# Performance work log

Hardware: AMD Instinct MI355X
Metric: run time of the kernel (lower is better)

## Reference

```python
import jax, jax.numpy as jnp
import numpy as np
import math

D_MODEL = 1024
N_HEADS = 16
D_HEAD = 64


def setup_inputs() -> dict:
    key = jax.random.key(0)
    ks = jax.random.split(key, 9)
    B, T = 2, 2048
    s = 1.0 / math.sqrt(D_MODEL)
    return {
        "x": jax.random.normal(ks[0], (B, T, D_MODEL), dtype=jnp.float32),
        "Wq": jax.random.normal(ks[1], (D_MODEL, D_MODEL), dtype=jnp.float32) * s,
        "bq": jnp.zeros((D_MODEL,), dtype=jnp.float32),
        "Wk": jax.random.normal(ks[2], (D_MODEL, D_MODEL), dtype=jnp.float32) * s,
        "bk": jnp.zeros((D_MODEL,), dtype=jnp.float32),
        "Wv": jax.random.normal(ks[3], (D_MODEL, D_MODEL), dtype=jnp.float32) * s,
        "bv": jnp.zeros((D_MODEL,), dtype=jnp.float32),
        "Wo": jax.random.normal(ks[4], (D_MODEL, D_MODEL), dtype=jnp.float32) * s,
        "bo": jnp.zeros((D_MODEL,), dtype=jnp.float32),
    }


def reference(x, Wq, bq, Wk, bk, Wv, bv, Wo, bo):
    B, T, _ = x.shape
    # Linear layers (torch convention: y = x @ W^T + b)
    Q = x @ Wq.T + bq
    K = x @ Wk.T + bk
    V = x @ Wv.T + bv
    # [B, H, T, Dh]
    Q = Q.reshape(B, T, N_HEADS, D_HEAD).transpose(0, 2, 1, 3)
    K = K.reshape(B, T, N_HEADS, D_HEAD).transpose(0, 2, 1, 3)
    V = V.reshape(B, T, N_HEADS, D_HEAD).transpose(0, 2, 1, 3)
    scores = jnp.einsum("bhqd,bhkd->bhqk", Q, K) / math.sqrt(D_HEAD)
    causal_mask = jnp.tril(jnp.ones((T, T), dtype=bool))  # [T, T]
    scores = jnp.where(causal_mask, scores, -jnp.inf)
    attn = jax.nn.softmax(scores, axis=-1)
    out = jnp.einsum("bhqk,bhkd->bhqd", attn, V)
    out = out.transpose(0, 2, 1, 3).reshape(B, T, D_MODEL)
    return out @ Wo.T + bo
```

## Files before the change

kernel.cpp:

```cpp
#include <hip/hip_runtime.h>

typedef unsigned short u16;
typedef __bf16 bf16x8 __attribute__((ext_vector_type(8)));
typedef float f32x4 __attribute__((ext_vector_type(4)));
typedef float f32x16 __attribute__((ext_vector_type(16)));
typedef u16 u16x4 __attribute__((ext_vector_type(4)));
typedef unsigned int uint;

#define DM 1024
#define MROWS 4096
#define TSEQ 2048

static __device__ __forceinline__ u16 f2b(float f) {
  uint u = __builtin_bit_cast(uint, f);
  uint r = (u + 0x7fffu + ((u >> 16) & 1u)) >> 16;
  return (u16)r;
}

static __device__ __forceinline__ uint pkbf(float a, float b) {
  union { __bf16 h[2]; uint u; } x;
  x.h[0] = (__bf16)a; x.h[1] = (__bf16)b;
  return x.u;
}

__global__ __launch_bounds__(256) void cvt_kernel(const float* __restrict__ in,
                                                  u16* __restrict__ out, int n,
                                                  float scale) {
  int i = (blockIdx.x * 256 + threadIdx.x) * 4;
  if (i >= n) return;
  float4 v = *(const float4*)(in + i);
  u16x4 o;
  o.x = f2b(v.x * scale); o.y = f2b(v.y * scale);
  o.z = f2b(v.z * scale); o.w = f2b(v.w * scale);
  *(u16x4*)(out + i) = o;
}

__global__ __launch_bounds__(256) void cvt4_kernel(
    const float* __restrict__ w0, const float* __restrict__ w1,
    const float* __restrict__ w2, const float* __restrict__ w3,
    u16* __restrict__ o0, u16* __restrict__ o1, u16* __restrict__ o2,
    u16* __restrict__ o3, float s0) {
  const int sel = blockIdx.y;
  const float* in = (sel == 0) ? w0 : (sel == 1) ? w1 : (sel == 2) ? w2 : w3;
  u16* out = (sel == 0) ? o0 : (sel == 1) ? o1 : (sel == 2) ? o2 : o3;
  const float scale = (sel == 0) ? s0 : 1.0f;
  int i = (blockIdx.x * 256 + threadIdx.x) * 4;
  float4 v = *(const float4*)(in + i);
  u16x4 o;
  o.x = f2b(v.x * scale); o.y = f2b(v.y * scale);
  o.z = f2b(v.z * scale); o.w = f2b(v.w * scale);
  *(u16x4*)(out + i) = o;
}

#define SWZ(o) ((o) ^ ((((o) >> 7) & 3) << 4))

static __device__ __forceinline__ void gemm_tile(const u16* __restrict__ A,
                                                 const u16* __restrict__ W,
                                                 int row0, int col0,
                                                 char* lds,
                                                 f32x4 (&acc)[4][4]) {
  const int tid = threadIdx.x;
  const int lane = tid & 63, wid = tid >> 6;
  const int wr = wid >> 1, wc = wid & 1;
  const int lg = lane >> 4, lr = lane & 15;

  const u16* srcA[2]; const u16* srcB[2]; int dst[2];
#pragma unroll
  for (int c = 0; c < 2; ++c) {
    int lin = (c * 256 + tid) * 16;
    int p = SWZ(lin);
    srcA[c] = A + (size_t)(row0 + (p >> 6)) * DM + ((p & 63) >> 1);
    srcB[c] = W + (size_t)(col0 + (p >> 6)) * DM + ((p & 63) >> 1);
    dst[c] = lin;
  }
  int offA[4], offB[4];
#pragma unroll
  for (int m = 0; m < 4; ++m) offA[m] = SWZ((wr * 64 + m * 16 + lr) * 64 + lg * 16);
#pragma unroll
  for (int n = 0; n < 4; ++n) offB[n] = SWZ((wc * 64 + n * 16 + lr) * 64 + lg * 16);

  f32x4 z = {0.f, 0.f, 0.f, 0.f};
#pragma unroll
  for (int m = 0; m < 4; ++m)
#pragma unroll
    for (int n = 0; n < 4; ++n) acc[m][n] = z;

  auto stage = [&](int k0, int buf) {
    char* bA = lds + buf * 16384;
    char* bB = bA + 8192;
#pragma unroll
    for (int c = 0; c < 2; ++c) {
      __builtin_amdgcn_global_load_lds(
          (const __attribute__((address_space(1))) void*)(srcA[c] + k0),
          (__attribute__((address_space(3))) void*)(bA + dst[c]), 16, 0, 0);
      __builtin_amdgcn_global_load_lds(
          (const __attribute__((address_space(1))) void*)(srcB[c] + k0),
          (__attribute__((address_space(3))) void*)(bB + dst[c]), 16, 0, 0);
    }
  };

  stage(0, 0);
  __syncthreads();
  int cur = 0;
  for (int k0 = 0; k0 < DM; k0 += 32) {
    if (k0 + 32 < DM) stage(k0 + 32, cur ^ 1);
    char* bA = lds + cur * 16384;
    char* bB = bA + 8192;
    bf16x8 av[4], bv[4];
#pragma unroll
    for (int m = 0; m < 4; ++m) av[m] = *(const bf16x8*)(bA + offA[m]);
#pragma unroll
    for (int n = 0; n < 4; ++n) bv[n] = *(const bf16x8*)(bB + offB[n]);
    __builtin_amdgcn_s_setprio(1);
#pragma unroll
    for (int m = 0; m < 4; ++m)
#pragma unroll
      for (int n = 0; n < 4; ++n)
        acc[m][n] = __builtin_amdgcn_mfma_f32_16x16x32_bf16(av[m], bv[n], acc[m][n], 0, 0, 0);
    __builtin_amdgcn_s_setprio(0);
    __syncthreads();
    cur ^= 1;
  }
}

__global__ __launch_bounds__(256) void qkv_gemm(
    const u16* __restrict__ xb, const u16* __restrict__ Wqb,
    const u16* __restrict__ Wkb, const u16* __restrict__ Wvb,
    const float* __restrict__ bq, const float* __restrict__ bk,
    const float* __restrict__ bv, u16* __restrict__ Qx, u16* __restrict__ Kx,
    u16* __restrict__ Vx) {
  __shared__ char lds[32768];
  const int seg = blockIdx.x >> 3, nt = blockIdx.x & 7;
  const int row0 = blockIdx.y * 128, col0 = nt * 128;
  const u16* W = (seg == 0) ? Wqb : (seg == 1) ? Wkb : Wvb;
  const float* bias = (seg == 0) ? bq : (seg == 1) ? bk : bv;
  const float bscale = (seg == 0) ? 0.18033688011112042f : 1.0f;

  f32x4 acc[4][4];
  gemm_tile(xb, W, row0, col0, lds, acc);

  const int tid = threadIdx.x;
  const int lane = tid & 63, wid = tid >> 6;
  const int wr = wid >> 1, wc = wid & 1;
  const int lg = lane >> 4, lr = lane & 15;

  float bcol[4];
#pragma unroll
  for (int n = 0; n < 4; ++n) bcol[n] = bias[col0 + wc * 64 + n * 16 + lr] * bscale;
#pragma unroll
  for (int m = 0; m < 4; ++m)
#pragma unroll
    for (int n = 0; n < 4; ++n) {
      int colB = (wc * 64 + n * 16 + lr) * 2;
#pragma unroll
      for (int r = 0; r < 4; ++r) {
        int row = wr * 64 + m * 16 + lg * 4 + r;
        *(u16*)(lds + row * 256 + (colB ^ ((row & 7) << 4))) =
            f2b(acc[m][n][r] + bcol[n]);
      }
    }
  __syncthreads();

  const int st = tid >> 5, lnq = tid & 31;
  const int bI = row0 >> 11;
  if (seg < 2) {
    u16* out = (seg == 0) ? Qx : Kx;
    const int hloc = st & 1, twloc = st >> 1;
    const int h = (col0 >> 6) + hloc;
    const int tw = ((row0 & 2047) >> 5) + twloc;
    u16* base = out + ((size_t)(bI * 16 + h) * 64 + tw) * 2048;
#pragma unroll
    for (int ch = 0; ch < 8; ++ch) {
      int q = ch * 256 + lnq * 8;
      int c = q >> 9, hi2 = (q >> 8) & 1;
      int row = twloc * 32 + lnq;
      int colB = hloc * 128 + c * 32 + hi2 * 16;
      bf16x8 v = *(const bf16x8*)(lds + row * 256 + (colB ^ ((row & 7) << 4)));
      *(bf16x8*)(base + q) = v;
    }
  } else {
    const int hloc = st & 1, ktloc = st >> 1;
    const int h = (col0 >> 6) + hloc;
    const int kt = ((row0 & 2047) >> 5) + ktloc;
    u16* base = Vx + ((size_t)(bI * 16 + h) * 64 + kt) * 2048;
#pragma unroll
    for (int ch = 0; ch < 8; ++ch) {
      int q = ch * 256 + lnq * 8;
      int hi2 = ch & 1, hh = (ch >> 1) & 1, c = (ch >> 2) & 1;
      int colB = (hloc * 64 + hh * 32 + lnq) * 2;
      union { u16 a[8]; bf16x8 v; } t;
#pragma unroll
      for (int j = 0; j < 8; ++j) {
        int kvi = 16 * c + (j & 3) + 8 * (j >> 2) + 4 * hi2;
        int row = ktloc * 32 + kvi;
        t.a[j] = *(const u16*)(lds + row * 256 + (colB ^ ((row & 7) << 4)));
      }
      *(bf16x8*)(base + q) = t.v;
    }
  }
}

__global__ __launch_bounds__(256, 4) void attn_kernel(const u16* __restrict__ Qx,
                                                      const u16* __restrict__ Kx,
                                                      const u16* __restrict__ Vx,
                                                      u16* __restrict__ Aout) {
  __shared__ u16 stg[2][2][4096];
  __shared__ float mml[2][64][2];
  const int tid = threadIdx.x, lane = tid & 63, wid = tid >> 6;
  const int hi = lane >> 5, ln = lane & 31;
  const int half = wid & 1, spl = wid >> 1;
  const int id = blockIdx.x + (blockIdx.y << 5);
  const int xcd = id & 7, idx = id >> 3;
  const int bh = xcd * 4 + (idx & 3);
  const int qt = 31 - (idx >> 2);
  const int b = bh >> 4, h = bh & 15;
  const int q0 = qt * 64 + half * 32;
  const int tbeg = spl * (qt + 1);
  const int tend = tbeg + (qt + 1);

  const u16* Qp = Qx + ((size_t)bh * 64 + (q0 >> 5)) * 2048;
  const u16* Kt = Kx + (size_t)bh * 64 * 2048;
  const u16* Vt = Vx + (size_t)bh * 64 * 2048;

  bf16x8 qf[4];
#pragma unroll
  for (int c = 0; c < 4; ++c)
    qf[c] = *(const bf16x8*)(Qp + c * 512 + hi * 256 + ln * 8);

  f32x16 Oa, Ob;
#pragma unroll
  for (int r = 0; r < 16; ++r) { Oa[r] = 0.f; Ob[r] = 0.f; }
  float m = -1e30f, l = 0.f;

  u16* myStg = &stg[spl][0][0];
  const u16* srcB = (half == 0) ? Kt : Vt;
  auto stage = [&](int kt, int s) {
    const u16* src = srcB + (size_t)kt * 2048;
    u16* dst = myStg + s * 4096 + half * 2048;
#pragma unroll
    for (int c = 0; c < 4; ++c)
      __builtin_amdgcn_global_load_lds(
          (const __attribute__((address_space(1))) void*)(src + c * 512 + lane * 8),
          (__attribute__((address_space(3))) void*)(dst + c * 512 + lane * 8),
          16, 0, 0);
  };

  stage(tbeg, 0);
  __syncthreads();
  for (int kt = tbeg; kt < tend; ++kt) {
    const int s = (kt - tbeg) & 1;
    if (kt + 1 < tend) stage(kt + 1, s ^ 1);
    const u16* Kl = myStg + s * 4096;
    const u16* Vl = Kl + 2048;
    bf16x8 kf[4], vf[4];
#pragma unroll
    for (int c = 0; c < 4; ++c)
      kf[c] = *(const bf16x8*)(Kl + c * 512 + hi * 256 + ln * 8);
#pragma unroll
    for (int c = 0; c < 4; ++c)
      vf[c] = *(const bf16x8*)(Vl + c * 512 + hi * 256 + ln * 8);
    f32x16 S;
#pragma unroll
    for (int r = 0; r < 16; ++r) S[r] = 0.f;
    __builtin_amdgcn_s_setprio(1);
#pragma unroll
    for (int c = 0; c < 4; ++c)
      S = __builtin_amdgcn_mfma_f32_32x32x16_bf16(kf[c], qf[c], S, 0, 0, 0);
    __builtin_amdgcn_s_setprio(0);
    if (kt >= (q0 >> 5)) {
      const int q = q0 + ln;
#pragma unroll
      for (int r = 0; r < 16; ++r) {
        int kv = kt * 32 + (r & 3) + 8 * (r >> 2) + 4 * hi;
        if (kv > q) S[r] = -1e38f;
      }
    }
    float a0 = fmaxf(fmaxf(S[0], S[1]), S[2]);
    float a1 = fmaxf(fmaxf(S[3], S[4]), S[5]);
    float a2 = fmaxf(fmaxf(S[6], S[7]), S[8]);
    float a3 = fmaxf(fmaxf(S[9], S[10]), S[11]);
    float a4 = fmaxf(fmaxf(S[12], S[13]), S[14]);
    float mx = fmaxf(fmaxf(fmaxf(a0, a1), fmaxf(a2, a3)), fmaxf(a4, S[15]));
    if (!__all(mx - m <= 8.f)) {
      float nm = fmaxf(m, mx);
      nm = fmaxf(nm, __shfl_xor(nm, 32));
      float sf = __builtin_amdgcn_exp2f(m - nm);
      m = nm; l *= sf;
#pragma unroll
      for (int r = 0; r < 16; ++r) { Oa[r] *= sf; Ob[r] *= sf; }
    }
#pragma unroll
    for (int r = 0; r < 16; ++r) S[r] = __builtin_amdgcn_exp2f(S[r] - m);
    float ts = ((S[0] + S[1]) + (S[2] + S[3])) + ((S[4] + S[5]) + (S[6] + S[7]));
    ts += ((S[8] + S[9]) + (S[10] + S[11])) + ((S[12] + S[13]) + (S[14] + S[15]));
    l += ts;
    uint pw[8];
#pragma unroll
    for (int i = 0; i < 8; ++i) pw[i] = pkbf(S[2 * i], S[2 * i + 1]);
    __builtin_amdgcn_s_setprio(1);
#pragma unroll
    for (int c = 0; c < 2; ++c) {
      union { uint w[4]; bf16x8 v; } pf;
      pf.w[0] = pw[4 * c + 0]; pf.w[1] = pw[4 * c + 1];
      pf.w[2] = pw[4 * c + 2]; pf.w[3] = pw[4 * c + 3];
      Oa = __builtin_amdgcn_mfma_f32_32x32x16_bf16(vf[2 * c + 0], pf.v, Oa, 0, 0, 0);
      Ob = __builtin_amdgcn_mfma_f32_32x32x16_bf16(vf[2 * c + 1], pf.v, Ob, 0, 0, 0);
    }
    __builtin_amdgcn_s_setprio(0);
    __syncthreads();
  }

  union uo { f32x16 v; f32x4 q[4]; };
  const int sw8 = lane & 7;
  char* moc = (char*)&stg[0][0][0] + half * 8192;
  if (spl == 1) {
    uo ua, ub; ua.v = Oa; ub.v = Ob;
#pragma unroll
    for (int c = 0; c < 4; ++c) {
      *(f32x4*)(moc + lane * 128 + ((c ^ sw8) * 16)) = ua.q[c];
      *(f32x4*)(moc + lane * 128 + (((c + 4) ^ sw8) * 16)) = ub.q[c];
    }
    mml[half][lane][0] = m;
    mml[half][lane][1] = l;
  }
  __syncthreads();
  if (spl == 1) return;

  {
    float mY = mml[half][lane][0], lY = mml[half][lane][1];
    f32x4 rb[8];
#pragma unroll
    for (int c = 0; c < 8; ++c)
      rb[c] = *(const f32x4*)(moc + lane * 128 + ((c ^ sw8) * 16));
    float M = fmaxf(m, mY);
    float eX = __builtin_amdgcn_exp2f(m - M);
    float eY = __builtin_amdgcn_exp2f(mY - M);
    uo ua, ub; ua.v = Oa; ub.v = Ob;
#pragma unroll
    for (int c = 0; c < 4; ++c) {
      ua.q[c] = ua.q[c] * eX + rb[c] * eY;
      ub.q[c] = ub.q[c] * eX + rb[c + 4] * eY;
    }
    Oa = ua.v; Ob = ub.v;
    l = l * eX + lY * eY;
  }

  float lr = l + __shfl_xor(l, 32);
  const float inv = 1.f / lr;

  __threadfence_block();
  char* Tc = moc;
#pragma unroll
  for (int i = 0; i < 8; ++i) {
    int d0 = (2 * i & 3) + 8 * ((2 * i) >> 2) + 4 * hi;
    uint wA = pkbf(Oa[2 * i] * inv, Oa[2 * i + 1] * inv);
    *(uint*)(Tc + (ln * 128 + ((d0 * 2) ^ ((ln & 7) << 4)))) = wA;
    uint wB = pkbf(Ob[2 * i] * inv, Ob[2 * i + 1] * inv);
    *(uint*)(Tc + (ln * 128 + (((d0 + 32) * 2) ^ ((ln & 7) << 4)))) = wB;
  }
  __threadfence_block();
  u16* Ap = Aout + (size_t)b * TSEQ * DM + h * 64 + (size_t)(q0 + ln) * DM;
#pragma unroll
  for (int j = 0; j < 4; ++j) {
    int oct = hi * 4 + j;
    bf16x8 v = *(const bf16x8*)(Tc + (ln * 128 + ((oct * 16) ^ ((ln & 7) << 4))));
    *(bf16x8*)(Ap + oct * 8) = v;
  }
}

__global__ __launch_bounds__(256) void out_gemm(const u16* __restrict__ attn,
                                                const u16* __restrict__ Wob,
                                                const float* __restrict__ bo,
                                                float* __restrict__ out) {
  __shared__ char lds[32768];
  const int row0 = blockIdx.y * 128, col0 = blockIdx.x * 128;
  f32x4 acc[4][4];
  gemm_tile(attn, Wob, row0, col0, lds, acc);

  const int tid = threadIdx.x;
  const int lane = tid & 63, wid = tid >> 6;
  const int wr = wid >> 1, wc = wid & 1;
  const int lg = lane >> 4, lr = lane & 15;
#pragma unroll
  for (int m = 0; m < 4; ++m)
#pragma unroll
    for (int n = 0; n < 4; ++n) {
      int col = col0 + wc * 64 + n * 16 + lr;
      float b = bo[col];
#pragma unroll
      for (int r = 0; r < 4; ++r) {
        int row = row0 + wr * 64 + m * 16 + lg * 4 + r;
        out[(size_t)row * DM + col] = acc[m][n][r] + b;
      }
    }
}

extern "C" void kernel_launch(void* const* d_in, const int* in_sizes, int n_in,
                              void* d_out, int out_size, void* d_ws, size_t ws_size,
                              hipStream_t stream) {
  const float* x = (const float*)d_in[0];
  const float* Wq = (const float*)d_in[1];
  const float* bq = (const float*)d_in[2];
  const float* Wk = (const float*)d_in[3];
  const float* bk = (const float*)d_in[4];
  const float* Wv = (const float*)d_in[5];
  const float* bv = (const float*)d_in[6];
  const float* Wo = (const float*)d_in[7];
  const float* bo = (const float*)d_in[8];

  char* ws = (char*)d_ws;
  const size_t MB = 1024 * 1024;
  u16* xb = (u16*)(ws);
  u16* Wqb = (u16*)(ws + 8 * MB);
  u16* Wkb = (u16*)(ws + 10 * MB);
  u16* Wvb = (u16*)(ws + 12 * MB);
  u16* Wob = (u16*)(ws + 14 * MB);
  u16* Qf = (u16*)(ws + 16 * MB);
  u16* Kf = (u16*)(ws + 24 * MB);
  u16* Vf = (u16*)(ws + 32 * MB);
  u16* attnb = xb;

  cvt_kernel<<<4096, 256, 0, stream>>>(x, xb, MROWS * DM, 1.0f);
  cvt4_kernel<<<dim3(1024, 4), 256, 0, stream>>>(Wq, Wk, Wv, Wo, Wqb, Wkb, Wvb,
                                                 Wob, 0.18033688011112042f);

  qkv_gemm<<<dim3(24, 32), 256, 0, stream>>>(xb, Wqb, Wkb, Wvb, bq, bk, bv, Qf, Kf, Vf);
  attn_kernel<<<dim3(32, 32), 256, 0, stream>>>(Qf, Kf, Vf, attnb);
  out_gemm<<<dim3(8, 32), 256, 0, stream>>>(attnb, Wob, bo, (float*)d_out);
}
```

Before: 101.0 us.

## Merge conversion kernels, vectorize V transpose, and register-prefetch K/V in attention

The two fp32-to-bf16 conversion launches become one kernel, removing a launch. In the QKV GEMM epilogue, V is written to LDS directly in its transposed, swizzled layout so the scattered 2-byte reads become single 16-byte reads. The attention kernel drops the shared LDS staging and per-tile __syncthreads, and instead loads K and V tiles straight into registers with double-buffered K prefetch. It also splits the KV range per 32-row half rather than per 64-row tile, which balances causal work and applies the mask only on the diagonal tile, at the cost of more register pressure and uncoalesced-reuse global loads.

```diff
diff --git a/kernel.cpp b/kernel.cpp
--- a/kernel.cpp
+++ b/kernel.cpp
@@ -23,28 +23,23 @@
   return x.u;
 }
 
-__global__ __launch_bounds__(256) void cvt_kernel(const float* __restrict__ in,
-                                                  u16* __restrict__ out, int n,
-                                                  float scale) {
-  int i = (blockIdx.x * 256 + threadIdx.x) * 4;
-  if (i >= n) return;
-  float4 v = *(const float4*)(in + i);
-  u16x4 o;
-  o.x = f2b(v.x * scale); o.y = f2b(v.y * scale);
-  o.z = f2b(v.z * scale); o.w = f2b(v.w * scale);
-  *(u16x4*)(out + i) = o;
-}
-
-__global__ __launch_bounds__(256) void cvt4_kernel(
-    const float* __restrict__ w0, const float* __restrict__ w1,
-    const float* __restrict__ w2, const float* __restrict__ w3,
-    u16* __restrict__ o0, u16* __restrict__ o1, u16* __restrict__ o2,
-    u16* __restrict__ o3, float s0) {
-  const int sel = blockIdx.y;
-  const float* in = (sel == 0) ? w0 : (sel == 1) ? w1 : (sel == 2) ? w2 : w3;
-  u16* out = (sel == 0) ? o0 : (sel == 1) ? o1 : (sel == 2) ? o2 : o3;
-  const float scale = (sel == 0) ? s0 : 1.0f;
-  int i = (blockIdx.x * 256 + threadIdx.x) * 4;
+__global__ __launch_bounds__(256) void cvt_all(
+    const float* __restrict__ x, const float* __restrict__ w0,
+    const float* __restrict__ w1, const float* __restrict__ w2,
+    const float* __restrict__ w3, u16* __restrict__ xo, u16* __restrict__ o0,
+    u16* __restrict__ o1, u16* __restrict__ o2, u16* __restrict__ o3,
+    float s0) {
+  const int bid = blockIdx.x;
+  const float* in; u16* out; float scale = 1.0f; int i;
+  if (bid < 4096) {
+    in = x; out = xo; i = bid * 1024 + threadIdx.x * 4;
+  } else {
+    int sel = (bid - 4096) >> 10;
+    in = (sel == 0) ? w0 : (sel == 1) ? w1 : (sel == 2) ? w2 : w3;
+    out = (sel == 0) ? o0 : (sel == 1) ? o1 : (sel == 2) ? o2 : o3;
+    if (sel == 0) scale = s0;
+    i = ((bid - 4096) & 1023) * 1024 + threadIdx.x * 4;
+  }
   float4 v = *(const float4*)(in + i);
   u16x4 o;
   o.x = f2b(v.x * scale); o.y = f2b(v.y * scale);
@@ -147,18 +142,43 @@
   float bcol[4];
 #pragma unroll
   for (int n = 0; n < 4; ++n) bcol[n] = bias[col0 + wc * 64 + n * 16 + lr] * bscale;
-#pragma unroll
-  for (int m = 0; m < 4; ++m)
-#pragma unroll
-    for (int n = 0; n < 4; ++n) {
-      int colB = (wc * 64 + n * 16 + lr) * 2;
-#pragma unroll
-      for (int r = 0; r < 4; ++r) {
-        int row = wr * 64 + m * 16 + lg * 4 + r;
-        *(u16*)(lds + row * 256 + (colB ^ ((row & 7) << 4))) =
-            f2b(acc[m][n][r] + bcol[n]);
+
+  if (seg < 2) {
+#pragma unroll
+    for (int m = 0; m < 4; ++m)
+#pragma unroll
+      for (int n = 0; n < 4; ++n) {
+        int colB = (wc * 64 + n * 16 + lr) * 2;
+#pragma unroll
+        for (int r = 0; r < 4; ++r) {
+          int row = wr * 64 + m * 16 + lg * 4 + r;
+          *(u16*)(lds + row * 256 + (colB ^ ((row & 7) << 4))) =
+              f2b(acc[m][n][r] + bcol[n]);
+        }
       }
-    }
+  } else {
+    const int hi2 = lg & 1, jh = lg >> 1;
+#pragma unroll
+    for (int m = 0; m < 4; ++m) {
+      const int c = m & 1;
+      const int ktl = wr * 2 + (m >> 1);
+#pragma unroll
+      for (int n = 0; n < 4; ++n) {
+        int col = wc * 64 + n * 16 + lr;
+        int hloc = col >> 6, dcol = col & 63;
+        int hh = dcol >> 5, dp = dcol & 31;
+        int byte = (hloc * 4 + ktl) * 4096 + (((c * 2 + hh) * 2 + hi2) * 512) +
+                   dp * 16 + jh * 8;
+        byte ^= ((dp & 3) << 5) ^ (hi2 << 6);
+        u16x4 pk;
+        pk.x = f2b(acc[m][n][0] + bcol[n]);
+        pk.y = f2b(acc[m][n][1] + bcol[n]);
+        pk.z = f2b(acc[m][n][2] + bcol[n]);
+        pk.w = f2b(acc[m][n][3] + bcol[n]);
+        *(u16x4*)(lds + byte) = pk;
+      }
+    }
+  }
   __syncthreads();
 
   const int st = tid >> 5, lnq = tid & 31;
@@ -179,23 +199,17 @@
       *(bf16x8*)(base + q) = v;
     }
   } else {
-    const int hloc = st & 1, ktloc = st >> 1;
+    const int hloc = st & 1, ktl = st >> 1;
     const int h = (col0 >> 6) + hloc;
-    const int kt = ((row0 & 2047) >> 5) + ktloc;
+    const int kt = ((row0 & 2047) >> 5) + ktl;
     u16* base = Vx + ((size_t)(bI * 16 + h) * 64 + kt) * 2048;
 #pragma unroll
     for (int ch = 0; ch < 8; ++ch) {
-      int q = ch * 256 + lnq * 8;
-      int hi2 = ch & 1, hh = (ch >> 1) & 1, c = (ch >> 2) & 1;
-      int colB = (hloc * 64 + hh * 32 + lnq) * 2;
-      union { u16 a[8]; bf16x8 v; } t;
-#pragma unroll
-      for (int j = 0; j < 8; ++j) {
-        int kvi = 16 * c + (j & 3) + 8 * (j >> 2) + 4 * hi2;
-        int row = ktloc * 32 + kvi;
-        t.a[j] = *(const u16*)(lds + row * 256 + (colB ^ ((row & 7) << 4)));
-      }
-      *(bf16x8*)(base + q) = t.v;
+      int hi2 = ch & 1;
+      int byte = (hloc * 4 + ktl) * 4096 + ch * 512 + lnq * 16;
+      byte ^= ((lnq & 3) << 5) ^ (hi2 << 6);
+      bf16x8 v = *(const bf16x8*)(lds + byte);
+      *(bf16x8*)(base + ch * 256 + lnq * 8) = v;
     }
   }
 }
@@ -204,7 +218,7 @@
                                                       const u16* __restrict__ Kx,
                                                       const u16* __restrict__ Vx,
                                                       u16* __restrict__ Aout) {
-  __shared__ u16 stg[2][2][4096];
+  __shared__ float mrg[2][64][32];
   __shared__ float mml[2][64][2];
   const int tid = threadIdx.x, lane = tid & 63, wid = tid >> 6;
   const int hi = lane >> 5, ln = lane & 31;
@@ -215,8 +229,10 @@
   const int qt = 31 - (idx >> 2);
   const int b = bh >> 4, h = bh & 15;
   const int q0 = qt * 64 + half * 32;
-  const int tbeg = spl * (qt + 1);
-  const int tend = tbeg + (qt + 1);
+  const int ntile = (q0 >> 5) + 1;
+  const int halfn = (ntile + 1) >> 1;
+  const int tbeg = spl ? halfn : 0;
+  const int tend = spl ? ntile : halfn;
 
   const u16* Qp = Qx + ((size_t)bh * 64 + (q0 >> 5)) * 2048;
   const u16* Kt = Kx + (size_t)bh * 64 * 2048;
@@ -232,33 +248,20 @@
   for (int r = 0; r < 16; ++r) { Oa[r] = 0.f; Ob[r] = 0.f; }
   float m = -1e30f, l = 0.f;
 
-  u16* myStg = &stg[spl][0][0];
-  const u16* srcB = (half == 0) ? Kt : Vt;
-  auto stage = [&](int kt, int s) {
-    const u16* src = srcB + (size_t)kt * 2048;
-    u16* dst = myStg + s * 4096 + half * 2048;
+  bf16x8 kA[4], kB[4], vf[4];
+  auto loadK = [&](int kt, bf16x8 (&kf)[4]) {
+    const u16* Kp = Kt + (size_t)kt * 2048;
 #pragma unroll
     for (int c = 0; c < 4; ++c)
-      __builtin_amdgcn_global_load_lds(
-          (const __attribute__((address_space(1))) void*)(src + c * 512 + lane * 8),
-          (__attribute__((address_space(3))) void*)(dst + c * 512 + lane * 8),
-          16, 0, 0);
+      kf[c] = *(const bf16x8*)(Kp + c * 512 + hi * 256 + ln * 8);
   };
-
-  stage(tbeg, 0);
-  __syncthreads();
-  for (int kt = tbeg; kt < tend; ++kt) {
-    const int s = (kt - tbeg) & 1;
-    if (kt + 1 < tend) stage(kt + 1, s ^ 1);
-    const u16* Kl = myStg + s * 4096;
-    const u16* Vl = Kl + 2048;
-    bf16x8 kf[4], vf[4];
+  auto loadV = [&](int kt) {
+    const u16* Vp = Vt + (size_t)kt * 2048;
 #pragma unroll
     for (int c = 0; c < 4; ++c)
-      kf[c] = *(const bf16x8*)(Kl + c * 512 + hi * 256 + ln * 8);
-#pragma unroll
-    for (int c = 0; c < 4; ++c)
-      vf[c] = *(const bf16x8*)(Vl + c * 512 + hi * 256 + ln * 8);
+      vf[c] = *(const bf16x8*)(Vp + c * 512 + hi * 256 + ln * 8);
+  };
+  auto tile = [&](const bf16x8 (&kf)[4], int kt) {
     f32x16 S;
 #pragma unroll
     for (int r = 0; r < 16; ++r) S[r] = 0.f;
@@ -267,7 +270,7 @@
     for (int c = 0; c < 4; ++c)
       S = __builtin_amdgcn_mfma_f32_32x32x16_bf16(kf[c], qf[c], S, 0, 0, 0);
     __builtin_amdgcn_s_setprio(0);
-    if (kt >= (q0 >> 5)) {
+    if (kt == ntile - 1) {
       const int q = q0 + ln;
 #pragma unroll
       for (int r = 0; r < 16; ++r) {
@@ -307,12 +310,23 @@
       Ob = __builtin_amdgcn_mfma_f32_32x32x16_bf16(vf[2 * c + 1], pf.v, Ob, 0, 0, 0);
     }
     __builtin_amdgcn_s_setprio(0);
-    __syncthreads();
-  }
+  };
+
+  if (tbeg < tend) loadK(tbeg, kA);
+  int kt = tbeg;
+  for (; kt + 2 <= tend; kt += 2) {
+    loadV(kt);
+    loadK(kt + 1, kB);
+    tile(kA, kt);
+    loadV(kt + 1);
+    if (kt + 2 < tend) loadK(kt + 2, kA);
+    tile(kB, kt + 1);
+  }
+  if (kt < tend) { loadV(kt); tile(kA, kt); }
 
   union uo { f32x16 v; f32x4 q[4]; };
   const int sw8 = lane & 7;
-  char* moc = (char*)&stg[0][0][0] + half * 8192;
+  char* moc = (char*)&mrg[half][0][0];
   if (spl == 1) {
     uo ua, ub; ua.v = Oa; ub.v = Ob;
 #pragma unroll
@@ -420,9 +434,8 @@
   u16* Vf = (u16*)(ws + 32 * MB);
   u16* attnb = xb;
 
-  cvt_kernel<<<4096, 256, 0, stream>>>(x, xb, MROWS * DM, 1.0f);
-  cvt4_kernel<<<dim3(1024, 4), 256, 0, stream>>>(Wq, Wk, Wv, Wo, Wqb, Wkb, Wvb,
-                                                 Wob, 0.18033688011112042f);
+  cvt_all<<<8192, 256, 0, stream>>>(x, Wq, Wk, Wv, Wo, xb, Wqb, Wkb, Wvb, Wob,
+                                    0.18033688011112042f);
 
   qkv_gemm<<<dim3(24, 32), 256, 0, stream>>>(xb, Wqb, Wkb, Wvb, bq, bk, bv, Qf, Kf, Vf);
   attn_kernel<<<dim3(32, 32), 256, 0, stream>>>(Qf, Kf, Vf, attnb);
```

Measured after the change: 134.9 us. 1.34x slower.
